# Kernel optimization log

Measured on AMD Instinct MI355X. Metric: run time of the kernel, lower is better.

Reference implementation:

```python
import jax, jax.numpy as jnp
import numpy as np

H = 512      # hidden size
V = 10000    # input_output_size (vocab)
L = 32       # max_length
B = 256      # batch
SOS = 1


def setup_inputs() -> dict:
    key = jax.random.key(0)
    ks = jax.random.split(key, 20)
    g = lambda k, shape: jax.random.normal(k, shape, dtype=jnp.float32) * 0.05
    return dict(
        input_tensor=jax.random.randint(ks[0], (B, L), 0, V),
        target_tensor=jax.random.randint(ks[1], (B, L), 0, V),
        # encoder: embedding + GRU
        enc_embed=g(ks[2], (V, H)),
        enc_w_ih=g(ks[3], (3 * H, H)), enc_w_hh=g(ks[4], (3 * H, H)),
        enc_b_ih=g(ks[5], (3 * H,)), enc_b_hh=g(ks[6], (3 * H,)),
        # attention decoder: embedding + attn + attn_combine + GRU + out
        dec_embed=g(ks[7], (V, H)),
        attn_w=g(ks[8], (L, 2 * H)), attn_b=g(ks[9], (L,)),
        comb_w=g(ks[10], (H, 2 * H)), comb_b=g(ks[11], (H,)),
        dec_w_ih=g(ks[12], (3 * H, H)), dec_w_hh=g(ks[13], (3 * H, H)),
        dec_b_ih=g(ks[14], (3 * H,)), dec_b_hh=g(ks[15], (3 * H,)),
        out_w=g(ks[16], (V, H)), out_b=g(ks[17], (V,)),
    )


def _gru_step(x, h, w_ih, w_hh, b_ih, b_hh):
    # PyTorch GRUCell math. x, h: [B, H]
    gi = x @ w_ih.T + b_ih          # [B, 3H]
    gh = h @ w_hh.T + b_hh          # [B, 3H]
    i_r, i_z, i_n = jnp.split(gi, 3, axis=-1)
    h_r, h_z, h_n = jnp.split(gh, 3, axis=-1)
    r = jax.nn.sigmoid(i_r + h_r)
    z = jax.nn.sigmoid(i_z + h_z)
    n = jnp.tanh(i_n + r * h_n)
    return (1.0 - z) * n + z * h


def reference(input_tensor, target_tensor,
              enc_embed, enc_w_ih, enc_w_hh, enc_b_ih, enc_b_hh,
              dec_embed, attn_w, attn_b, comb_w, comb_b,
              dec_w_ih, dec_w_hh, dec_b_ih, dec_b_hh, out_w, out_b):
    inp_t = input_tensor.T   # [L, B]
    tgt_t = target_tensor.T  # [L, B]
    h0 = jnp.zeros((B, H), dtype=enc_embed.dtype)

    # ---- encoder: scan over time ----
    def enc_step(h, tok):
        x = enc_embed[tok]  # [B, H]
        h2 = _gru_step(x, h, enc_w_ih, enc_w_hh, enc_b_ih, enc_b_hh)
        return h2, h2       # encoder output == hidden

    enc_hidden, enc_outs = jax.lax.scan(enc_step, h0, inp_t)  # enc_outs: [L, B, H]

    # ---- decoder with teacher forcing (phase='train', ratio=1.0) ----
    sos = jnp.full((1, B), SOS, dtype=tgt_t.dtype)
    dec_inputs = jnp.concatenate([sos, tgt_t[:-1]], axis=0)  # [L, B]

    def dec_step(h, tok):
        emb = dec_embed[tok]                                   # [B, H]
        aw = jax.nn.softmax(jnp.concatenate([emb, h], axis=-1) @ attn_w.T + attn_b)  # [B, L]
        applied = jnp.einsum('bl,lbh->bh', aw, enc_outs)       # attention over encoder outputs
        x = jax.nn.relu(jnp.concatenate([emb, applied], axis=-1) @ comb_w.T + comb_b)
        h2 = _gru_step(x, h, dec_w_ih, dec_w_hh, dec_b_ih, dec_b_hh)
        logits = jax.nn.log_softmax(h2 @ out_w.T + out_b)      # [B, V]
        return h2, logits

    _, network_outputs = jax.lax.scan(dec_step, enc_hidden, dec_inputs)  # [L, B, V]
    return network_outputs
```

## Files before the change

### kernel.cpp

```cpp
#include <hip/hip_runtime.h>

#define HD 512
#define VOC 10000
#define SL 32
#define BA 256
#define BH (BA*HD)

typedef __bf16 b16x8 __attribute__((ext_vector_type(8)));
typedef float f32x4 __attribute__((ext_vector_type(4)));
typedef unsigned u32x4 __attribute__((ext_vector_type(4)));

__device__ __forceinline__ ushort f2bf(float x) {
  unsigned u = __float_as_uint(x);
  u += 0x7fffu + ((u >> 16) & 1u);
  return (ushort)(u >> 16);
}

__device__ __forceinline__ void stg_sc(void* p, u32x4 v) {
  asm volatile("global_store_dwordx4 %0, %1, off sc0 sc1"
               :: "v"(p), "v"(v) : "memory");
}
__device__ __forceinline__ void stg_sc1(void* p, unsigned v) {
  asm volatile("global_store_dword %0, %1, off sc0 sc1"
               :: "v"(p), "v"(v) : "memory");
}
__device__ __forceinline__ void stg_plain(void* p, unsigned v) {
  asm volatile("global_store_dword %0, %1, off"
               :: "v"(p), "v"(v) : "memory");
}
__device__ __forceinline__ unsigned ldg_sc0(const void* p) {
  unsigned v;
  asm volatile("global_load_dword %0, %1, off sc0"
               : "=v"(v) : "v"(p) : "memory");
  asm volatile("s_waitcnt vmcnt(0)" ::: "memory");
  return v;
}
__device__ __forceinline__ unsigned ldg_sc1(const void* p) {
  unsigned v;
  asm volatile("global_load_dword %0, %1, off sc0 sc1"
               : "=v"(v) : "v"(p) : "memory");
  asm volatile("s_waitcnt vmcnt(0)" ::: "memory");
  return v;
}
__device__ __forceinline__ void vmwait0() {
  asm volatile("s_waitcnt vmcnt(0)" ::: "memory");
  __builtin_amdgcn_sched_barrier(0);
}

__global__ __launch_bounds__(256) void cvt3_k(
    const float* __restrict__ w_out, ushort* __restrict__ o_out,
    const float* __restrict__ w_comb, ushort* __restrict__ o_comb,
    const float* __restrict__ w_attn, ushort* __restrict__ o_attn) {
  int b = blockIdx.x;
  const float* in; ushort* out; int i; int n4;
  if (b < 5000)      { in = w_out;  out = o_out;  i = b * 256 + threadIdx.x;          n4 = 1280000; }
  else if (b < 5512) { in = w_comb; out = o_comb; i = (b - 5000) * 256 + threadIdx.x; n4 = 131072; }
  else               { in = w_attn; out = o_attn; i = (b - 5512) * 256 + threadIdx.x; n4 = 8192; }
  if (i < n4) {
    float4 v = ((const float4*)in)[i];
    ((ushort4*)out)[i] = make_ushort4(f2bf(v.x), f2bf(v.y), f2bf(v.z), f2bf(v.w));
  }
}

__global__ __launch_bounds__(64) void gather2_k(
    const float* __restrict__ enc_t, const float* __restrict__ dec_t,
    const int* __restrict__ in_tok, const int* __restrict__ tgt_tok,
    ushort* __restrict__ enc_o, ushort* __restrict__ dec_o) {
  int bid = blockIdx.x;
  int isDec = bid >= SL * BA;
  int row = isDec ? bid - SL * BA : bid;
  int l = row >> 8, b = row & 255;
  int tok = isDec ? ((l == 0) ? 1 : tgt_tok[b * SL + l - 1]) : in_tok[b * SL + l];
  const float* table = isDec ? dec_t : enc_t;
  ushort* out = isDec ? dec_o : enc_o;
  const float4* src = (const float4*)(table + (size_t)tok * HD);
  int t = threadIdx.x;
  float4 v0 = src[t * 2], v1 = src[t * 2 + 1];
  uint4 o;
  o.x = (unsigned)f2bf(v0.x) | ((unsigned)f2bf(v0.y) << 16);
  o.y = (unsigned)f2bf(v0.z) | ((unsigned)f2bf(v0.w) << 16);
  o.z = (unsigned)f2bf(v1.x) | ((unsigned)f2bf(v1.y) << 16);
  o.w = (unsigned)f2bf(v1.z) | ((unsigned)f2bf(v1.w) << 16);
  *(uint4*)(out + (size_t)row * HD + t * 8) = o;
}

__global__ __launch_bounds__(256) void gemm_k(
    const ushort* __restrict__ A, const ushort* __restrict__ W,
    int N, int ldw, const float* __restrict__ bias,
    float* __restrict__ outf, int ldc) {
  __shared__ ushort lsA[4][64][8];
  __shared__ ushort lsB[4][64][8];
  __shared__ float ctile[64][68];
  int t = threadIdx.x;
  int lane = t & 63, w = t >> 6;
  int m0 = blockIdx.x * 64, n0 = blockIdx.y * 64;
  f32x4 acc[4] = {};
  int sr = t >> 2, g = t & 3;
  const ushort* Ap = A + (size_t)(m0 + sr) * HD + g * 8;
  int nr = n0 + sr; if (nr > N - 1) nr = N - 1;
  const ushort* Wp = W + (size_t)nr * ldw + g * 8;
  for (int ks = 0; ks < 16; ++ks) {
    *(uint4*)(&lsA[g][sr][0]) = *(const uint4*)(Ap + ks * 32);
    *(uint4*)(&lsB[g][sr][0]) = *(const uint4*)(Wp + ks * 32);
    __syncthreads();
    int gg = lane >> 4, r = lane & 15;
    b16x8 bf = *(const b16x8*)(&lsB[gg][w * 16 + r][0]);
#pragma unroll
    for (int mi = 0; mi < 4; ++mi) {
      b16x8 af = *(const b16x8*)(&lsA[gg][mi * 16 + r][0]);
      acc[mi] = __builtin_amdgcn_mfma_f32_16x16x32_bf16(af, bf, acc[mi], 0, 0, 0);
    }
    __syncthreads();
  }
  int gg = lane >> 4, cl = lane & 15;
  int tcol = w * 16 + cl;
  int bc = n0 + tcol; if (bc > N - 1) bc = N - 1;
  float bv = bias ? bias[bc] : 0.f;
#pragma unroll
  for (int mi = 0; mi < 4; ++mi)
#pragma unroll
    for (int r = 0; r < 4; ++r)
      ctile[mi * 16 + gg * 4 + r][tcol] = acc[mi][r] + bv;
  __syncthreads();
  int row = t >> 2, q = t & 3;
#pragma unroll
  for (int j = 0; j < 4; ++j) {
    int c = q * 16 + j * 4;
    if (n0 + c + 3 <= N - 1)
      *(float4*)(outf + (size_t)(m0 + row) * ldc + n0 + c) =
          *(const float4*)&ctile[row][c];
  }
}

__global__ __launch_bounds__(256) void gemmW_k(
    const ushort* __restrict__ A, const ushort* __restrict__ W,
    ushort* __restrict__ outS) {
  __shared__ ushort lsA[4][64][8];
  __shared__ ushort lsB[4][64][8];
  __shared__ ushort ctileS[64][64];
  int t = threadIdx.x, lane = t & 63, w = t >> 6;
  int m0 = blockIdx.x * 64, n0 = blockIdx.y * 64;
  f32x4 acc[4] = {};
  int sr = t >> 2, g = t & 3;
  const ushort* Ap = A + (size_t)(m0 + sr) * HD + g * 8;
  const ushort* Wp = W + (size_t)(n0 + sr) * 1024 + 512 + g * 8;
  for (int ks = 0; ks < 16; ++ks) {
    *(uint4*)(&lsA[g][sr][0]) = *(const uint4*)(Ap + ks * 32);
    *(uint4*)(&lsB[g][sr][0]) = *(const uint4*)(Wp + ks * 32);
    __syncthreads();
    int gg = lane >> 4, r = lane & 15;
    b16x8 bf = *(const b16x8*)(&lsB[gg][w * 16 + r][0]);
#pragma unroll
    for (int mi = 0; mi < 4; ++mi) {
      b16x8 af = *(const b16x8*)(&lsA[gg][mi * 16 + r][0]);
      acc[mi] = __builtin_amdgcn_mfma_f32_16x16x32_bf16(af, bf, acc[mi], 0, 0, 0);
    }
    __syncthreads();
  }
  int gg = lane >> 4, cl = lane & 15;
  int tcol = w * 16 + cl;
#pragma unroll
  for (int mi = 0; mi < 4; ++mi)
#pragma unroll
    for (int r = 0; r < 4; ++r)
      ctileS[mi * 16 + gg * 4 + r][tcol] = f2bf(acc[mi][r]);
  __syncthreads();
  int l = m0 >> 8, b0 = m0 & 255;
  int sl_i = t >> 6, tid = t & 63;
  ushort* dst = outS + (((size_t)l * 32 + (n0 >> 4) + sl_i) * 256 + b0 + tid) * 16;
  *(uint4*)dst = *(const uint4*)&ctileS[tid][sl_i * 16];
  *(uint4*)(dst + 8) = *(const uint4*)&ctileS[tid][sl_i * 16 + 8];
}

__global__ __launch_bounds__(256) void gemm128_k(
    const ushort* __restrict__ A, const ushort* __restrict__ W,
    int N, const float* __restrict__ bias,
    float* __restrict__ outf, int ldc) {
  __shared__ ushort lsA[4][128][8];
  __shared__ ushort lsB[4][64][8];
  __shared__ float ctile[128][68];
  int t = threadIdx.x, lane = t & 63, w = t >> 6;
  int m0 = blockIdx.x * 128, n0 = blockIdx.y * 64;
  f32x4 acc[8] = {};
  int arow = t >> 1, ag = t & 1;
  const ushort* Ap = A + (size_t)(m0 + arow) * HD + ag * 16;
  int brow = t >> 2, bg = t & 3;
  int nr = n0 + brow; if (nr > N - 1) nr = N - 1;
  const ushort* Wp = W + (size_t)nr * HD + bg * 8;
  for (int ks = 0; ks < 16; ++ks) {
    *(uint4*)(&lsA[ag * 2][arow][0])     = *(const uint4*)(Ap + ks * 32);
    *(uint4*)(&lsA[ag * 2 + 1][arow][0]) = *(const uint4*)(Ap + ks * 32 + 8);
    *(uint4*)(&lsB[bg][brow][0])         = *(const uint4*)(Wp + ks * 32);
    __syncthreads();
    int gg = lane >> 4, r = lane & 15;
    b16x8 bf = *(const b16x8*)(&lsB[gg][w * 16 + r][0]);
#pragma unroll
    for (int mi = 0; mi < 8; ++mi) {
      b16x8 af = *(const b16x8*)(&lsA[gg][mi * 16 + r][0]);
      acc[mi] = __builtin_amdgcn_mfma_f32_16x16x32_bf16(af, bf, acc[mi], 0, 0, 0);
    }
    __syncthreads();
  }
  int gg = lane >> 4, cl = lane & 15;
  int tcol = w * 16 + cl;
  int bc = n0 + tcol; if (bc > N - 1) bc = N - 1;
  float bv = bias[bc];
#pragma unroll
  for (int mi = 0; mi < 8; ++mi)
#pragma unroll
    for (int r = 0; r < 4; ++r)
      ctile[mi * 16 + gg * 4 + r][tcol] = acc[mi][r] + bv;
  __syncthreads();
  int row = t >> 1, hf = t & 1;
#pragma unroll
  for (int j = 0; j < 8; ++j) {
    int c = hf * 32 + j * 4;
    if (n0 + c + 3 <= N - 1)
      *(float4*)(outf + (size_t)(m0 + row) * ldc + n0 + c) =
          *(const float4*)&ctile[row][c];
  }
}


__device__ __forceinline__ const ushort* sfrag(const ushort* base, int kh,
                                               int gg, int row) {
  return base + (kh * 16 + (gg >> 1)) * 4096 + row * 16 + (gg & 1) * 8;
}

template <bool XS>
__device__ __forceinline__ void gru_phase(
    int r0, int sl, int lane, int w, int t,
    const ushort* __restrict__ x_src, const ushort* __restrict__ h_src,
    const ushort (*Wlds)[2][8][64][8],
    const float* __restrict__ b_ih, const float* __restrict__ b_hh,
    float* hp, ushort* __restrict__ hbf_dst, ushort* __restrict__ hrm_dst,
    float (*red)[6][64][4], ushort (*stile)[16]) {
  int mf = w & 1, kh = w >> 1;
  int lr = lane & 15, gg = lane >> 4;
  int row_a = r0 + mf * 16 + lr;
  b16x8 xa[8], ha[8];
  if (XS) {
    const ushort* xr = sfrag(x_src, kh, gg, row_a);
#pragma unroll
    for (int ks = 0; ks < 8; ++ks) xa[ks] = *(const b16x8*)(xr + ks * 8192);
  } else {
    const ushort* xr = x_src + (size_t)row_a * HD + kh * 256 + gg * 8;
#pragma unroll
    for (int ks = 0; ks < 8; ++ks) xa[ks] = *(const b16x8*)(xr + ks * 32);
  }
  if (h_src) {
    const ushort* hr = sfrag(h_src, kh, gg, row_a);
#pragma unroll
    for (int ks = 0; ks < 8; ++ks) ha[ks] = *(const b16x8*)(hr + ks * 8192);
  } else {
#pragma unroll
    for (int ks = 0; ks < 8; ++ks) ha[ks] = b16x8{};
  }
  f32x4 acc[6] = {};
#pragma unroll
  for (int ks = 0; ks < 8; ++ks) {
#pragma unroll
    for (int g3 = 0; g3 < 3; ++g3) {
      b16x8 bi = *(const b16x8*)(&Wlds[g3][kh][ks][lane][0]);
      b16x8 bh = *(const b16x8*)(&Wlds[3 + g3][kh][ks][lane][0]);
      acc[g3] = __builtin_amdgcn_mfma_f32_16x16x32_bf16(xa[ks], bi, acc[g3], 0, 0, 0);
      acc[3 + g3] = __builtin_amdgcn_mfma_f32_16x16x32_bf16(ha[ks], bh, acc[3 + g3], 0, 0, 0);
    }
  }
  if (kh == 1) {
#pragma unroll
    for (int s = 0; s < 6; ++s) *(f32x4*)&red[mf][s][lane][0] = acc[s];
  }
  __syncthreads();
  if (kh == 0) {
    int j = sl * 16 + lr;
#pragma unroll
    for (int s = 0; s < 6; ++s) acc[s] += *(const f32x4*)&red[mf][s][lane][0];
    float bir = b_ih[j], biz = b_ih[512 + j], bin_ = b_ih[1024 + j];
    float bhr = b_hh[j], bhz = b_hh[512 + j], bhn = b_hh[1024 + j];
#pragma unroll
    for (int ri = 0; ri < 4; ++ri) {
      float ir = acc[0][ri] + bir, iz = acc[1][ri] + biz, inn = acc[2][ri] + bin_;
      float hr2 = acc[3][ri] + bhr, hz = acc[4][ri] + bhz, hn = acc[5][ri] + bhn;
      float rr = 1.f / (1.f + expf(-(ir + hr2)));
      float zz = 1.f / (1.f + expf(-(iz + hz)));
      float nn = tanhf(inn + rr * hn);
      float h2 = (1.f - zz) * nn + zz * hp[ri];
      hp[ri] = h2;
      stile[mf * 16 + gg * 4 + ri][lr] = f2bf(h2);
    }
  }
  __syncthreads();
  if (t < 64) {
    stg_sc(hbf_dst + sl * 4096 + r0 * 16 + t * 8, ((const u32x4*)stile)[t]);
    int row = t >> 1, c = t & 1;
    *(uint4*)(hrm_dst + (size_t)(r0 + row) * HD + sl * 16 + c * 8) =
        *(const uint4*)&stile[row][c * 8];
  }
}

__device__ __forceinline__ void attnx_phase(
    int r0, int sl, int lane, int w, int t, int l,
    const ushort* __restrict__ h_bf, const ushort* __restrict__ attn_w_bf,
    const float* __restrict__ attn_pre, const ushort* __restrict__ encW,
    const float* __restrict__ comb_pre, ushort* __restrict__ x_dst,
    float (*sS)[32][33], float (*sAW)[33], ushort (*stile)[16]) {
  int mf = w & 1, kh = w >> 1;
  int lr = lane & 15, gg = lane >> 4;
  int row_a = r0 + mf * 16 + lr;
  const ushort* hr = sfrag(h_bf, kh, gg, row_a);
  const ushort* w0 = attn_w_bf + (size_t)lr * 1024 + 512 + kh * 256 + gg * 8;
  const ushort* w1 = attn_w_bf + (size_t)(16 + lr) * 1024 + 512 + kh * 256 + gg * 8;
  f32x4 a0 = {}, a1 = {};
#pragma unroll
  for (int ks = 0; ks < 8; ++ks) {
    b16x8 ah = *(const b16x8*)(hr + ks * 8192);
    b16x8 b0 = *(const b16x8*)(w0 + ks * 32);
    b16x8 b1 = *(const b16x8*)(w1 + ks * 32);
    a0 = __builtin_amdgcn_mfma_f32_16x16x32_bf16(ah, b0, a0, 0, 0, 0);
    a1 = __builtin_amdgcn_mfma_f32_16x16x32_bf16(ah, b1, a1, 0, 0, 0);
  }
#pragma unroll
  for (int ri = 0; ri < 4; ++ri) {
    sS[kh][mf * 16 + gg * 4 + ri][lr] = a0[ri];
    sS[kh][mf * 16 + gg * 4 + ri][16 + lr] = a1[ri];
  }
  __syncthreads();
  int r = t >> 3, q = t & 7;
  float4 pre = *(const float4*)(attn_pre + ((size_t)l * BA + r0 + r) * 32 + q * 4);
  float v0 = sS[0][r][q * 4 + 0] + sS[1][r][q * 4 + 0] + pre.x;
  float v1 = sS[0][r][q * 4 + 1] + sS[1][r][q * 4 + 1] + pre.y;
  float v2 = sS[0][r][q * 4 + 2] + sS[1][r][q * 4 + 2] + pre.z;
  float v3 = sS[0][r][q * 4 + 3] + sS[1][r][q * 4 + 3] + pre.w;
  float mx = fmaxf(fmaxf(v0, v1), fmaxf(v2, v3));
  for (int o = 1; o < 8; o <<= 1) mx = fmaxf(mx, __shfl_xor(mx, o, 64));
  float e0 = expf(v0 - mx), e1 = expf(v1 - mx), e2 = expf(v2 - mx), e3 = expf(v3 - mx);
  float s = e0 + e1 + e2 + e3;
  for (int o = 1; o < 8; o <<= 1) s += __shfl_xor(s, o, 64);
  float inv = 1.f / s;
  sAW[r][q * 4 + 0] = e0 * inv; sAW[r][q * 4 + 1] = e1 * inv;
  sAW[r][q * 4 + 2] = e2 * inv; sAW[r][q * 4 + 3] = e3 * inv;
  __syncthreads();
  int rr = t >> 3, dp = t & 7;
  const float* cp = comb_pre + ((size_t)l * BA + r0 + rr) * HD + sl * 16 + dp * 2;
  float f0 = cp[0], f1 = cp[1];
  const ushort* ep = encW + sl * 4096 + (r0 + rr) * 16 + dp * 2;
#pragma unroll 8
  for (int ll = 0; ll < 32; ++ll) {
    float aw = sAW[rr][ll];
    unsigned u = *(const unsigned*)(ep + (size_t)ll * BH);
    f0 += aw * __uint_as_float(u << 16);
    f1 += aw * __uint_as_float(u & 0xffff0000u);
  }
  f0 = fmaxf(f0, 0.f); f1 = fmaxf(f1, 0.f);
  unsigned ov = (unsigned)f2bf(f0) | ((unsigned)f2bf(f1) << 16);
  *(unsigned*)&stile[rr][dp * 2] = ov;
  __syncthreads();
  if (t < 64)
    stg_sc(x_dst + sl * 4096 + r0 * 16 + t * 8, ((const u32x4*)stile)[t]);
}

struct EncArgs {
  const ushort* enc_emb_bf;
  const float* enc_w_ih; const float* enc_w_hh;
  const float* enc_b_ih; const float* enc_b_hh;
  ushort* enc_outs_s;
  ushort* enc_outs_rm;
  float* Hc;
  unsigned* fL2; unsigned* fLLC;
};

struct DecArgs {
  const float* dec_w_ih; const float* dec_w_hh;
  const float* dec_b_ih; const float* dec_b_hh;
  const ushort* attn_w_bf;
  const float* attn_pre;
  const float* comb_pre;
  const ushort* enc_outs_s;
  const ushort* encW;
  const float* Hc;
  ushort* H2_s; ushort* H2_rm; ushort* x_s;
  unsigned* fL2; unsigned* fLLC;
};

union DScr {
  float red[2][6][64][4];
  struct { float sS[2][32][33]; float sAW[32][33]; } at;
};

#define GSYNC_DEF(fL2p, fLLCp)                                          \
  auto gsync = [&]() {                                                  \
    ++sync_idx;                                                         \
    __syncthreads();                                                    \
    if (w == 0) {                                                       \
      vmwait0();                                                        \
      if (lane == 0) {                                                  \
        stg_plain(&(fL2p)[sl * 4], sync_idx);                           \
        stg_sc1(&(fLLCp)[sl * 16], sync_idx);                           \
      }                                                                 \
      int it = 0;                                                       \
      for (;;) {                                                        \
        unsigned v = ldg_sc0(&(fL2p)[(lane & 31) * 4]);                 \
        if (!__any(v < sync_idx)) break;                                \
        if ((++it & 3) == 0) {                                          \
          unsigned v2 = ldg_sc1(&(fLLCp)[(lane & 31) * 16]);            \
          if (!__any(v < sync_idx && v2 < sync_idx)) break;             \
        }                                                               \
        __builtin_amdgcn_s_sleep(1);                                    \
      }                                                                 \
    }                                                                   \
    __syncthreads();                                                    \
  }

#define LOAD_GRU_W32(Wih, Whh)                                          \
  for (int c = w; c < 96; c += 4) {                                     \
    int g = c >> 4, rem = c & 15, kh2 = rem >> 3, ks = rem & 7;         \
    const float* src = (g < 3) ? (Wih) : (Whh);                         \
    int gr = (g % 3) * 512 + sl * 16 + (lane & 15);                     \
    int col = kh2 * 256 + ks * 32 + (lane >> 4) * 8;                    \
    const float4* s4 = (const float4*)(src + (size_t)gr * HD + col);    \
    float4 va = s4[0], vb = s4[1];                                      \
    uint4 o;                                                            \
    o.x = (unsigned)f2bf(va.x) | ((unsigned)f2bf(va.y) << 16);          \
    o.y = (unsigned)f2bf(va.z) | ((unsigned)f2bf(va.w) << 16);          \
    o.z = (unsigned)f2bf(vb.x) | ((unsigned)f2bf(vb.y) << 16);          \
    o.w = (unsigned)f2bf(vb.z) | ((unsigned)f2bf(vb.w) << 16);          \
    *(uint4*)&Wlds[g][kh2][ks][lane][0] = o;                            \
  }

__global__ __launch_bounds__(256) void enc_k(EncArgs a) {
  __shared__ ushort Wlds[6][2][8][64][8];
  __shared__ float red[2][6][64][4];
  __shared__ ushort stile[32][16];
  int bid = blockIdx.x;
  int rg = bid & 7, sl = bid >> 3;
  int t = threadIdx.x, lane = t & 63, w = t >> 6;
  int r0 = rg * 32;
  unsigned* fL2 = a.fL2 + rg * 32 * 4;
  unsigned* fLLC = a.fLLC + rg * 32 * 16;
  unsigned sync_idx = 0;
  GSYNC_DEF(fL2, fLLC);

  LOAD_GRU_W32(a.enc_w_ih, a.enc_w_hh);
  __syncthreads();

  float hp[4] = {0.f, 0.f, 0.f, 0.f};
  for (int l = 0; l < SL; ++l) {
    gru_phase<false>(r0, sl, lane, w, t,
                     a.enc_emb_bf + (size_t)l * BH,
                     l ? a.enc_outs_s + (size_t)(l - 1) * BH : nullptr,
                     Wlds, a.enc_b_ih, a.enc_b_hh,
                     hp, a.enc_outs_s + (size_t)l * BH,
                     a.enc_outs_rm + (size_t)l * BH, red, stile);
    if (l != SL - 1) gsync();
  }
  if ((w >> 1) == 0) {
    int mf2 = w & 1, gg2 = lane >> 4, j = sl * 16 + (lane & 15);
#pragma unroll
    for (int ri = 0; ri < 4; ++ri)
      a.Hc[(size_t)(r0 + mf2 * 16 + gg2 * 4 + ri) * HD + j] = hp[ri];
  }
}

__global__ __launch_bounds__(256) void dec_k(DecArgs a) {
  __shared__ ushort Wlds[6][2][8][64][8];
  __shared__ DScr scr;
  __shared__ ushort stile[32][16];
  int bid = blockIdx.x;
  int rg = bid & 7, sl = bid >> 3;
  int t = threadIdx.x, lane = t & 63, w = t >> 6;
  int r0 = rg * 32;
  unsigned* fL2 = a.fL2 + rg * 32 * 4;
  unsigned* fLLC = a.fLLC + rg * 32 * 16;
  unsigned sync_idx = 0;
  GSYNC_DEF(fL2, fLLC);

  LOAD_GRU_W32(a.dec_w_ih, a.dec_w_hh);

  float hp[4] = {0.f, 0.f, 0.f, 0.f};
  if ((w >> 1) == 0) {
    int mf2 = w & 1, gg2 = lane >> 4, j = sl * 16 + (lane & 15);
#pragma unroll
    for (int ri = 0; ri < 4; ++ri)
      hp[ri] = a.Hc[(size_t)(r0 + mf2 * 16 + gg2 * 4 + ri) * HD + j];
  }
  __syncthreads();

  for (int l = 0; l < SL; ++l) {
    const ushort* h_bf = l ? a.H2_s + (size_t)(l - 1) * BH
                           : a.enc_outs_s + (size_t)31 * BH;
    attnx_phase(r0, sl, lane, w, t, l, h_bf, a.attn_w_bf, a.attn_pre,
                a.encW, a.comb_pre, a.x_s + (size_t)l * BH,
                scr.at.sS, scr.at.sAW, stile);
    gsync();
    gru_phase<true>(r0, sl, lane, w, t, a.x_s + (size_t)l * BH, h_bf,
                    Wlds, a.dec_b_ih, a.dec_b_hh,
                    hp, a.H2_s + (size_t)l * BH,
                    a.H2_rm + (size_t)l * BH, scr.red, stile);
    if (l != SL - 1) gsync();
  }
}

__global__ __launch_bounds__(256) void lsesub_k(float* __restrict__ logits) {
  __shared__ float redm[4], reds[4];
  int row = blockIdx.x, t = threadIdx.x;
  float4* p = (float4*)(logits + (size_t)row * VOC);
  float4 v[10];
  float m = -1e30f, s = 0.f;
#pragma unroll
  for (int j = 0; j < 10; ++j) {
    int i = t + j * 256;
    if (i < 2500) {
      v[j] = p[i];
      float mx = fmaxf(fmaxf(v[j].x, v[j].y), fmaxf(v[j].z, v[j].w));
      if (mx > m) { s *= expf(m - mx); m = mx; }
      s += expf(v[j].x - m) + expf(v[j].y - m) + expf(v[j].z - m) + expf(v[j].w - m);
    }
  }
#pragma unroll
  for (int o = 32; o; o >>= 1) {
    float m2 = __shfl_xor(m, o, 64), s2 = __shfl_xor(s, o, 64);
    float mn = fmaxf(m, m2);
    s = s * expf(m - mn) + s2 * expf(m2 - mn);
    m = mn;
  }
  if ((t & 63) == 0) { redm[t >> 6] = m; reds[t >> 6] = s; }
  __syncthreads();
  float mf = fmaxf(fmaxf(redm[0], redm[1]), fmaxf(redm[2], redm[3]));
  float sf = reds[0] * expf(redm[0] - mf) + reds[1] * expf(redm[1] - mf) +
             reds[2] * expf(redm[2] - mf) + reds[3] * expf(redm[3] - mf);
  float z = mf + logf(sf);
#pragma unroll
  for (int j = 0; j < 10; ++j) {
    int i = t + j * 256;
    if (i < 2500) {
      v[j].x -= z; v[j].y -= z; v[j].z -= z; v[j].w -= z;
      p[i] = v[j];
    }
  }
}

extern "C" void kernel_launch(void* const* d_in, const int* in_sizes, int n_in,
                              void* d_out, int out_size, void* d_ws, size_t ws_size,
                              hipStream_t stream) {
  (void)in_sizes; (void)n_in; (void)out_size; (void)ws_size;
  const int* in_tok = (const int*)d_in[0];
  const int* tgt_tok = (const int*)d_in[1];
  const float* enc_embed = (const float*)d_in[2];
  const float* enc_w_ih = (const float*)d_in[3];
  const float* enc_w_hh = (const float*)d_in[4];
  const float* enc_b_ih = (const float*)d_in[5];
  const float* enc_b_hh = (const float*)d_in[6];
  const float* dec_embed = (const float*)d_in[7];
  const float* attn_w = (const float*)d_in[8];
  const float* attn_b = (const float*)d_in[9];
  const float* comb_w = (const float*)d_in[10];
  const float* comb_b = (const float*)d_in[11];
  const float* dec_w_ih = (const float*)d_in[12];
  const float* dec_w_hh = (const float*)d_in[13];
  const float* dec_b_ih = (const float*)d_in[14];
  const float* dec_b_hh = (const float*)d_in[15];
  const float* out_w = (const float*)d_in[16];
  const float* out_b = (const float*)d_in[17];
  float* out = (float*)d_out;

  char* ws = (char*)d_ws;
  size_t off = 0;
  auto carve = [&](size_t bytes) {
    void* p = ws + off;
    off += (bytes + 255) & ~(size_t)255;
    return p;
  };
  ushort* comb_w_bf  = (ushort*)carve(512 * 1024 * 2);
  ushort* attn_w_bf  = (ushort*)carve(32 * 1024 * 2);
  ushort* out_w_bf   = (ushort*)carve((size_t)VOC * HD * 2);
  ushort* enc_emb_bf = (ushort*)carve((size_t)SL * BA * HD * 2);
  ushort* dec_emb_bf = (ushort*)carve((size_t)SL * BA * HD * 2);
  float* attn_pre    = (float*)carve((size_t)SL * BA * 32 * 4);
  float* comb_pre    = (float*)carve((size_t)SL * BA * HD * 4);
  ushort* enc_outs_s = (ushort*)carve((size_t)SL * BA * HD * 2);
  ushort* enc_outs_rm= (ushort*)carve((size_t)SL * BA * HD * 2);
  ushort* encW       = (ushort*)carve((size_t)SL * BA * HD * 2);
  ushort* H2_s       = (ushort*)carve((size_t)SL * BA * HD * 2);
  ushort* H2_rm      = (ushort*)carve((size_t)SL * BA * HD * 2);
  ushort* x_s        = (ushort*)carve((size_t)SL * BA * HD * 2);
  float* Hc          = (float*)carve((size_t)BA * HD * 4);
  unsigned* fE_L2    = (unsigned*)carve(8 * 32 * 4 * 4);
  unsigned* fE_LLC   = (unsigned*)carve(8 * 32 * 16 * 4);
  unsigned* fD_L2    = (unsigned*)carve(8 * 32 * 4 * 4);
  unsigned* fD_LLC   = (unsigned*)carve(8 * 32 * 16 * 4);

  hipMemsetAsync(fE_L2, 0, (8 * 32 * 4 + 8 * 32 * 16) * 2 * 4, stream);
  cvt3_k<<<5544, 256, 0, stream>>>(out_w, out_w_bf, comb_w, comb_w_bf,
                                   attn_w, attn_w_bf);
  gather2_k<<<2 * SL * BA, 64, 0, stream>>>(enc_embed, dec_embed, in_tok,
                                            tgt_tok, enc_emb_bf, dec_emb_bf);

  gemm_k<<<dim3(128, 1), 256, 0, stream>>>(dec_emb_bf, attn_w_bf, 32, 1024,
                                           attn_b, attn_pre, 32);
  gemm_k<<<dim3(128, 8), 256, 0, stream>>>(dec_emb_bf, comb_w_bf, 512, 1024,
                                           comb_b, comb_pre, 512);

  EncArgs ea;
  ea.enc_emb_bf = enc_emb_bf;
  ea.enc_w_ih = enc_w_ih; ea.enc_w_hh = enc_w_hh;
  ea.enc_b_ih = enc_b_ih; ea.enc_b_hh = enc_b_hh;
  ea.enc_outs_s = enc_outs_s;
  ea.enc_outs_rm = enc_outs_rm;
  ea.Hc = Hc;
  ea.fL2 = fE_L2; ea.fLLC = fE_LLC;
  void* ekargs[] = { (void*)&ea };
  hipError_t ce = hipLaunchCooperativeKernel(enc_k, dim3(256), dim3(256),
                                             ekargs, 0, stream);
  if (ce != hipSuccess) enc_k<<<256, 256, 0, stream>>>(ea);

  gemmW_k<<<dim3(128, 8), 256, 0, stream>>>(enc_outs_rm, comb_w_bf, encW);

  DecArgs da;
  da.dec_w_ih = dec_w_ih; da.dec_w_hh = dec_w_hh;
  da.dec_b_ih = dec_b_ih; da.dec_b_hh = dec_b_hh;
  da.attn_w_bf = attn_w_bf;
  da.attn_pre = attn_pre;
  da.comb_pre = comb_pre;
  da.enc_outs_s = enc_outs_s;
  da.encW = encW;
  da.Hc = Hc;
  da.H2_s = H2_s; da.H2_rm = H2_rm; da.x_s = x_s;
  da.fL2 = fD_L2; da.fLLC = fD_LLC;
  void* dkargs[] = { (void*)&da };
  ce = hipLaunchCooperativeKernel(dec_k, dim3(256), dim3(256),
                                  dkargs, 0, stream);
  if (ce != hipSuccess) dec_k<<<256, 256, 0, stream>>>(da);

  gemm128_k<<<dim3(64, 157), 256, 0, stream>>>(H2_rm, out_w_bf, VOC,
                                               out_b, out, VOC);
  lsesub_k<<<SL * BA, 256, 0, stream>>>(out);
}
```

Baseline: 893.4 us.

## Split grid barriers into produce/await and overlap independent GEMMs with waits

Replaces the monolithic grid sync with separate produce/await halves so each block can start work that does not depend on other blocks before it waits. In the encoder the input-side GRU GEMM runs before waiting on the previous hidden state. In the decoder the hidden-side GRU GEMM and the encW loads run before their waits. encW is re-laid out so each thread's 32 encoder timesteps are contiguous and can be prefetched into registers, and the two precompute GEMMs are merged into one launch. This cuts barrier stall time on the serial recurrence at the cost of more register pressure.

```diff
diff --git a/kernel.cpp b/kernel.cpp
--- a/kernel.cpp
+++ b/kernel.cpp
@@ -84,21 +84,26 @@
   *(uint4*)(out + (size_t)row * HD + t * 8) = o;
 }
 
-__global__ __launch_bounds__(256) void gemm_k(
-    const ushort* __restrict__ A, const ushort* __restrict__ W,
-    int N, int ldw, const float* __restrict__ bias,
-    float* __restrict__ outf, int ldc) {
+__global__ __launch_bounds__(256) void gemm2_k(
+    const ushort* __restrict__ A,
+    const ushort* __restrict__ Wc, const ushort* __restrict__ Wa,
+    const float* __restrict__ bc, const float* __restrict__ ba,
+    float* __restrict__ outc, float* __restrict__ outa) {
   __shared__ ushort lsA[4][64][8];
   __shared__ ushort lsB[4][64][8];
   __shared__ float ctile[64][68];
   int t = threadIdx.x;
   int lane = t & 63, w = t >> 6;
-  int m0 = blockIdx.x * 64, n0 = blockIdx.y * 64;
+  int by = blockIdx.y;
+  const ushort* W; const float* bias; float* outf; int N, n0, ldc;
+  if (by < 8) { W = Wc; bias = bc; outf = outc; N = 512; n0 = by * 64; ldc = 512; }
+  else        { W = Wa; bias = ba; outf = outa; N = 32;  n0 = 0;       ldc = 32; }
+  int m0 = blockIdx.x * 64;
   f32x4 acc[4] = {};
   int sr = t >> 2, g = t & 3;
   const ushort* Ap = A + (size_t)(m0 + sr) * HD + g * 8;
   int nr = n0 + sr; if (nr > N - 1) nr = N - 1;
-  const ushort* Wp = W + (size_t)nr * ldw + g * 8;
+  const ushort* Wp = W + (size_t)nr * 1024 + g * 8;
   for (int ks = 0; ks < 16; ++ks) {
     *(uint4*)(&lsA[g][sr][0]) = *(const uint4*)(Ap + ks * 32);
     *(uint4*)(&lsB[g][sr][0]) = *(const uint4*)(Wp + ks * 32);
@@ -114,8 +119,8 @@
   }
   int gg = lane >> 4, cl = lane & 15;
   int tcol = w * 16 + cl;
-  int bc = n0 + tcol; if (bc > N - 1) bc = N - 1;
-  float bv = bias ? bias[bc] : 0.f;
+  int bc2 = n0 + tcol; if (bc2 > N - 1) bc2 = N - 1;
+  float bv = bias[bc2];
 #pragma unroll
   for (int mi = 0; mi < 4; ++mi)
 #pragma unroll
@@ -134,7 +139,7 @@
 
 __global__ __launch_bounds__(256) void gemmW_k(
     const ushort* __restrict__ A, const ushort* __restrict__ W,
-    ushort* __restrict__ outS) {
+    ushort* __restrict__ outI) {
   __shared__ ushort lsA[4][64][8];
   __shared__ ushort lsB[4][64][8];
   __shared__ ushort ctileS[64][64];
@@ -167,7 +172,8 @@
   __syncthreads();
   int l = m0 >> 8, b0 = m0 & 255;
   int sl_i = t >> 6, tid = t & 63;
-  ushort* dst = outS + (((size_t)l * 32 + (n0 >> 4) + sl_i) * 256 + b0 + tid) * 16;
+  int sl_g = (n0 >> 4) + sl_i;
+  ushort* dst = outI + ((((size_t)sl_g * 256 + b0 + tid) * 32) + l) * 16;
   *(uint4*)dst = *(const uint4*)&ctileS[tid][sl_i * 16];
   *(uint4*)(dst + 8) = *(const uint4*)&ctileS[tid][sl_i * 16 + 8];
 }
@@ -227,139 +233,6 @@
   return base + (kh * 16 + (gg >> 1)) * 4096 + row * 16 + (gg & 1) * 8;
 }
 
-template <bool XS>
-__device__ __forceinline__ void gru_phase(
-    int r0, int sl, int lane, int w, int t,
-    const ushort* __restrict__ x_src, const ushort* __restrict__ h_src,
-    const ushort (*Wlds)[2][8][64][8],
-    const float* __restrict__ b_ih, const float* __restrict__ b_hh,
-    float* hp, ushort* __restrict__ hbf_dst, ushort* __restrict__ hrm_dst,
-    float (*red)[6][64][4], ushort (*stile)[16]) {
-  int mf = w & 1, kh = w >> 1;
-  int lr = lane & 15, gg = lane >> 4;
-  int row_a = r0 + mf * 16 + lr;
-  b16x8 xa[8], ha[8];
-  if (XS) {
-    const ushort* xr = sfrag(x_src, kh, gg, row_a);
-#pragma unroll
-    for (int ks = 0; ks < 8; ++ks) xa[ks] = *(const b16x8*)(xr + ks * 8192);
-  } else {
-    const ushort* xr = x_src + (size_t)row_a * HD + kh * 256 + gg * 8;
-#pragma unroll
-    for (int ks = 0; ks < 8; ++ks) xa[ks] = *(const b16x8*)(xr + ks * 32);
-  }
-  if (h_src) {
-    const ushort* hr = sfrag(h_src, kh, gg, row_a);
-#pragma unroll
-    for (int ks = 0; ks < 8; ++ks) ha[ks] = *(const b16x8*)(hr + ks * 8192);
-  } else {
-#pragma unroll
-    for (int ks = 0; ks < 8; ++ks) ha[ks] = b16x8{};
-  }
-  f32x4 acc[6] = {};
-#pragma unroll
-  for (int ks = 0; ks < 8; ++ks) {
-#pragma unroll
-    for (int g3 = 0; g3 < 3; ++g3) {
-      b16x8 bi = *(const b16x8*)(&Wlds[g3][kh][ks][lane][0]);
-      b16x8 bh = *(const b16x8*)(&Wlds[3 + g3][kh][ks][lane][0]);
-      acc[g3] = __builtin_amdgcn_mfma_f32_16x16x32_bf16(xa[ks], bi, acc[g3], 0, 0, 0);
-      acc[3 + g3] = __builtin_amdgcn_mfma_f32_16x16x32_bf16(ha[ks], bh, acc[3 + g3], 0, 0, 0);
-    }
-  }
-  if (kh == 1) {
-#pragma unroll
-    for (int s = 0; s < 6; ++s) *(f32x4*)&red[mf][s][lane][0] = acc[s];
-  }
-  __syncthreads();
-  if (kh == 0) {
-    int j = sl * 16 + lr;
-#pragma unroll
-    for (int s = 0; s < 6; ++s) acc[s] += *(const f32x4*)&red[mf][s][lane][0];
-    float bir = b_ih[j], biz = b_ih[512 + j], bin_ = b_ih[1024 + j];
-    float bhr = b_hh[j], bhz = b_hh[512 + j], bhn = b_hh[1024 + j];
-#pragma unroll
-    for (int ri = 0; ri < 4; ++ri) {
-      float ir = acc[0][ri] + bir, iz = acc[1][ri] + biz, inn = acc[2][ri] + bin_;
-      float hr2 = acc[3][ri] + bhr, hz = acc[4][ri] + bhz, hn = acc[5][ri] + bhn;
-      float rr = 1.f / (1.f + expf(-(ir + hr2)));
-      float zz = 1.f / (1.f + expf(-(iz + hz)));
-      float nn = tanhf(inn + rr * hn);
-      float h2 = (1.f - zz) * nn + zz * hp[ri];
-      hp[ri] = h2;
-      stile[mf * 16 + gg * 4 + ri][lr] = f2bf(h2);
-    }
-  }
-  __syncthreads();
-  if (t < 64) {
-    stg_sc(hbf_dst + sl * 4096 + r0 * 16 + t * 8, ((const u32x4*)stile)[t]);
-    int row = t >> 1, c = t & 1;
-    *(uint4*)(hrm_dst + (size_t)(r0 + row) * HD + sl * 16 + c * 8) =
-        *(const uint4*)&stile[row][c * 8];
-  }
-}
-
-__device__ __forceinline__ void attnx_phase(
-    int r0, int sl, int lane, int w, int t, int l,
-    const ushort* __restrict__ h_bf, const ushort* __restrict__ attn_w_bf,
-    const float* __restrict__ attn_pre, const ushort* __restrict__ encW,
-    const float* __restrict__ comb_pre, ushort* __restrict__ x_dst,
-    float (*sS)[32][33], float (*sAW)[33], ushort (*stile)[16]) {
-  int mf = w & 1, kh = w >> 1;
-  int lr = lane & 15, gg = lane >> 4;
-  int row_a = r0 + mf * 16 + lr;
-  const ushort* hr = sfrag(h_bf, kh, gg, row_a);
-  const ushort* w0 = attn_w_bf + (size_t)lr * 1024 + 512 + kh * 256 + gg * 8;
-  const ushort* w1 = attn_w_bf + (size_t)(16 + lr) * 1024 + 512 + kh * 256 + gg * 8;
-  f32x4 a0 = {}, a1 = {};
-#pragma unroll
-  for (int ks = 0; ks < 8; ++ks) {
-    b16x8 ah = *(const b16x8*)(hr + ks * 8192);
-    b16x8 b0 = *(const b16x8*)(w0 + ks * 32);
-    b16x8 b1 = *(const b16x8*)(w1 + ks * 32);
-    a0 = __builtin_amdgcn_mfma_f32_16x16x32_bf16(ah, b0, a0, 0, 0, 0);
-    a1 = __builtin_amdgcn_mfma_f32_16x16x32_bf16(ah, b1, a1, 0, 0, 0);
-  }
-#pragma unroll
-  for (int ri = 0; ri < 4; ++ri) {
-    sS[kh][mf * 16 + gg * 4 + ri][lr] = a0[ri];
-    sS[kh][mf * 16 + gg * 4 + ri][16 + lr] = a1[ri];
-  }
-  __syncthreads();
-  int r = t >> 3, q = t & 7;
-  float4 pre = *(const float4*)(attn_pre + ((size_t)l * BA + r0 + r) * 32 + q * 4);
-  float v0 = sS[0][r][q * 4 + 0] + sS[1][r][q * 4 + 0] + pre.x;
-  float v1 = sS[0][r][q * 4 + 1] + sS[1][r][q * 4 + 1] + pre.y;
-  float v2 = sS[0][r][q * 4 + 2] + sS[1][r][q * 4 + 2] + pre.z;
-  float v3 = sS[0][r][q * 4 + 3] + sS[1][r][q * 4 + 3] + pre.w;
-  float mx = fmaxf(fmaxf(v0, v1), fmaxf(v2, v3));
-  for (int o = 1; o < 8; o <<= 1) mx = fmaxf(mx, __shfl_xor(mx, o, 64));
-  float e0 = expf(v0 - mx), e1 = expf(v1 - mx), e2 = expf(v2 - mx), e3 = expf(v3 - mx);
-  float s = e0 + e1 + e2 + e3;
-  for (int o = 1; o < 8; o <<= 1) s += __shfl_xor(s, o, 64);
-  float inv = 1.f / s;
-  sAW[r][q * 4 + 0] = e0 * inv; sAW[r][q * 4 + 1] = e1 * inv;
-  sAW[r][q * 4 + 2] = e2 * inv; sAW[r][q * 4 + 3] = e3 * inv;
-  __syncthreads();
-  int rr = t >> 3, dp = t & 7;
-  const float* cp = comb_pre + ((size_t)l * BA + r0 + rr) * HD + sl * 16 + dp * 2;
-  float f0 = cp[0], f1 = cp[1];
-  const ushort* ep = encW + sl * 4096 + (r0 + rr) * 16 + dp * 2;
-#pragma unroll 8
-  for (int ll = 0; ll < 32; ++ll) {
-    float aw = sAW[rr][ll];
-    unsigned u = *(const unsigned*)(ep + (size_t)ll * BH);
-    f0 += aw * __uint_as_float(u << 16);
-    f1 += aw * __uint_as_float(u & 0xffff0000u);
-  }
-  f0 = fmaxf(f0, 0.f); f1 = fmaxf(f1, 0.f);
-  unsigned ov = (unsigned)f2bf(f0) | ((unsigned)f2bf(f1) << 16);
-  *(unsigned*)&stile[rr][dp * 2] = ov;
-  __syncthreads();
-  if (t < 64)
-    stg_sc(x_dst + sl * 4096 + r0 * 16 + t * 8, ((const u32x4*)stile)[t]);
-}
-
 struct EncArgs {
   const ushort* enc_emb_bf;
   const float* enc_w_ih; const float* enc_w_hh;
@@ -388,23 +261,26 @@
   struct { float sS[2][32][33]; float sAW[32][33]; } at;
 };
 
-#define GSYNC_DEF(fL2p, fLLCp)                                          \
-  auto gsync = [&]() {                                                  \
-    ++sync_idx;                                                         \
+#define BAR_DEFS(fL2p, fLLCp)                                           \
+  auto produce = [&](unsigned val) {                                    \
     __syncthreads();                                                    \
     if (w == 0) {                                                       \
       vmwait0();                                                        \
       if (lane == 0) {                                                  \
-        stg_plain(&(fL2p)[sl * 4], sync_idx);                           \
-        stg_sc1(&(fLLCp)[sl * 16], sync_idx);                           \
+        stg_plain(&(fL2p)[sl * 4], val);                                \
+        stg_sc1(&(fLLCp)[sl * 16], val);                                \
       }                                                                 \
+    }                                                                   \
+  };                                                                    \
+  auto await = [&](unsigned val) {                                      \
+    if (w == 0) {                                                       \
       int it = 0;                                                       \
       for (;;) {                                                        \
         unsigned v = ldg_sc0(&(fL2p)[(lane & 31) * 4]);                 \
-        if (!__any(v < sync_idx)) break;                                \
+        if (!__any(v < val)) break;                                     \
         if ((++it & 3) == 0) {                                          \
           unsigned v2 = ldg_sc1(&(fLLCp)[(lane & 31) * 16]);            \
-          if (!__any(v < sync_idx && v2 < sync_idx)) break;             \
+          if (!__any(v < val && v2 < val)) break;                       \
         }                                                               \
         __builtin_amdgcn_s_sleep(1);                                    \
       }                                                                 \
@@ -428,37 +304,100 @@
     *(uint4*)&Wlds[g][kh2][ks][lane][0] = o;                            \
   }
 
+#define GRU_TAIL(b_ih_, b_hh_, hbf_dst_, hrm_dst_)                      \
+  if (kh == 1) {                                                        \
+    _Pragma("unroll")                                                   \
+    for (int s = 0; s < 6; ++s) *(f32x4*)&redp[mf][s][lane][0] = acc[s];\
+  }                                                                     \
+  __syncthreads();                                                      \
+  if (kh == 0) {                                                        \
+    int j = sl * 16 + lr;                                               \
+    _Pragma("unroll")                                                   \
+    for (int s = 0; s < 6; ++s) acc[s] += *(const f32x4*)&redp[mf][s][lane][0]; \
+    float bir = (b_ih_)[j], biz = (b_ih_)[512 + j], bin_ = (b_ih_)[1024 + j]; \
+    float bhr = (b_hh_)[j], bhz = (b_hh_)[512 + j], bhn = (b_hh_)[1024 + j]; \
+    _Pragma("unroll")                                                   \
+    for (int ri = 0; ri < 4; ++ri) {                                    \
+      float ir = acc[0][ri] + bir, iz = acc[1][ri] + biz, inn = acc[2][ri] + bin_; \
+      float hr2 = acc[3][ri] + bhr, hz = acc[4][ri] + bhz, hn = acc[5][ri] + bhn; \
+      float rrg = 1.f / (1.f + expf(-(ir + hr2)));                      \
+      float zz = 1.f / (1.f + expf(-(iz + hz)));                        \
+      float nn = tanhf(inn + rrg * hn);                                 \
+      float h2 = (1.f - zz) * nn + zz * hp[ri];                         \
+      hp[ri] = h2;                                                      \
+      stile[mf * 16 + gg * 4 + ri][lr] = f2bf(h2);                      \
+    }                                                                   \
+  }                                                                     \
+  __syncthreads();                                                      \
+  if (t < 64) {                                                         \
+    stg_sc((hbf_dst_) + sl * 4096 + r0 * 16 + t * 8, ((const u32x4*)stile)[t]); \
+    if (hrm_dst_) {                                                     \
+      int row2 = t >> 1, c2 = t & 1;                                    \
+      *(uint4*)((hrm_dst_) + (size_t)(r0 + row2) * HD + sl * 16 + c2 * 8) = \
+          *(const uint4*)&stile[row2][c2 * 8];                          \
+    }                                                                   \
+  }
+
 __global__ __launch_bounds__(256) void enc_k(EncArgs a) {
   __shared__ ushort Wlds[6][2][8][64][8];
   __shared__ float red[2][6][64][4];
   __shared__ ushort stile[32][16];
+  float (*redp)[6][64][4] = red;
   int bid = blockIdx.x;
   int rg = bid & 7, sl = bid >> 3;
   int t = threadIdx.x, lane = t & 63, w = t >> 6;
   int r0 = rg * 32;
   unsigned* fL2 = a.fL2 + rg * 32 * 4;
   unsigned* fLLC = a.fLLC + rg * 32 * 16;
-  unsigned sync_idx = 0;
-  GSYNC_DEF(fL2, fLLC);
+  BAR_DEFS(fL2, fLLC);
 
   LOAD_GRU_W32(a.enc_w_ih, a.enc_w_hh);
   __syncthreads();
 
+  int mf = w & 1, kh = w >> 1;
+  int lr = lane & 15, gg = lane >> 4;
+  int row_a = r0 + mf * 16 + lr;
   float hp[4] = {0.f, 0.f, 0.f, 0.f};
+
   for (int l = 0; l < SL; ++l) {
-    gru_phase<false>(r0, sl, lane, w, t,
-                     a.enc_emb_bf + (size_t)l * BH,
-                     l ? a.enc_outs_s + (size_t)(l - 1) * BH : nullptr,
-                     Wlds, a.enc_b_ih, a.enc_b_hh,
-                     hp, a.enc_outs_s + (size_t)l * BH,
-                     a.enc_outs_rm + (size_t)l * BH, red, stile);
-    if (l != SL - 1) gsync();
+    const ushort* xr = a.enc_emb_bf + (size_t)l * BH + (size_t)row_a * HD +
+                       kh * 256 + gg * 8;
+    b16x8 xa[8];
+#pragma unroll
+    for (int ks = 0; ks < 8; ++ks) xa[ks] = *(const b16x8*)(xr + ks * 32);
+    f32x4 acc[6] = {};
+#pragma unroll
+    for (int ks = 0; ks < 8; ++ks)
+#pragma unroll
+      for (int g3 = 0; g3 < 3; ++g3)
+        acc[g3] = __builtin_amdgcn_mfma_f32_16x16x32_bf16(
+            xa[ks], *(const b16x8*)(&Wlds[g3][kh][ks][lane][0]), acc[g3], 0, 0, 0);
+    if (l) await((unsigned)l);
+    b16x8 ha[8];
+    if (l) {
+      const ushort* hr = sfrag(a.enc_outs_s + (size_t)(l - 1) * BH, kh, gg, row_a);
+#pragma unroll
+      for (int ks = 0; ks < 8; ++ks) ha[ks] = *(const b16x8*)(hr + ks * 8192);
+    } else {
+#pragma unroll
+      for (int ks = 0; ks < 8; ++ks) ha[ks] = b16x8{};
+    }
+#pragma unroll
+    for (int ks = 0; ks < 8; ++ks)
+#pragma unroll
+      for (int g3 = 0; g3 < 3; ++g3)
+        acc[3 + g3] = __builtin_amdgcn_mfma_f32_16x16x32_bf16(
+            ha[ks], *(const b16x8*)(&Wlds[3 + g3][kh][ks][lane][0]),
+            acc[3 + g3], 0, 0, 0);
+    GRU_TAIL(a.enc_b_ih, a.enc_b_hh, a.enc_outs_s + (size_t)l * BH,
+             a.enc_outs_rm + (size_t)l * BH);
+    if (l != SL - 1) produce((unsigned)(l + 1));
   }
   if ((w >> 1) == 0) {
-    int mf2 = w & 1, gg2 = lane >> 4, j = sl * 16 + (lane & 15);
+    int j = sl * 16 + lr;
 #pragma unroll
     for (int ri = 0; ri < 4; ++ri)
-      a.Hc[(size_t)(r0 + mf2 * 16 + gg2 * 4 + ri) * HD + j] = hp[ri];
+      a.Hc[(size_t)(r0 + mf * 16 + gg * 4 + ri) * HD + j] = hp[ri];
   }
 }
 
@@ -466,38 +405,128 @@
   __shared__ ushort Wlds[6][2][8][64][8];
   __shared__ DScr scr;
   __shared__ ushort stile[32][16];
+  float (*redp)[6][64][4] = scr.red;
   int bid = blockIdx.x;
   int rg = bid & 7, sl = bid >> 3;
   int t = threadIdx.x, lane = t & 63, w = t >> 6;
   int r0 = rg * 32;
   unsigned* fL2 = a.fL2 + rg * 32 * 4;
   unsigned* fLLC = a.fLLC + rg * 32 * 16;
-  unsigned sync_idx = 0;
-  GSYNC_DEF(fL2, fLLC);
+  BAR_DEFS(fL2, fLLC);
 
   LOAD_GRU_W32(a.dec_w_ih, a.dec_w_hh);
+
+  int mf = w & 1, kh = w >> 1;
+  int lr = lane & 15, gg = lane >> 4;
+  int row_a = r0 + mf * 16 + lr;
+  int rr = t >> 3, dp = t & 7;
 
   float hp[4] = {0.f, 0.f, 0.f, 0.f};
   if ((w >> 1) == 0) {
-    int mf2 = w & 1, gg2 = lane >> 4, j = sl * 16 + (lane & 15);
+    int j = sl * 16 + lr;
 #pragma unroll
     for (int ri = 0; ri < 4; ++ri)
-      hp[ri] = a.Hc[(size_t)(r0 + mf2 * 16 + gg2 * 4 + ri) * HD + j];
+      hp[ri] = a.Hc[(size_t)(r0 + mf * 16 + gg * 4 + ri) * HD + j];
   }
   __syncthreads();
 
   for (int l = 0; l < SL; ++l) {
     const ushort* h_bf = l ? a.H2_s + (size_t)(l - 1) * BH
                            : a.enc_outs_s + (size_t)31 * BH;
-    attnx_phase(r0, sl, lane, w, t, l, h_bf, a.attn_w_bf, a.attn_pre,
-                a.encW, a.comb_pre, a.x_s + (size_t)l * BH,
-                scr.at.sS, scr.at.sAW, stile);
-    gsync();
-    gru_phase<true>(r0, sl, lane, w, t, a.x_s + (size_t)l * BH, h_bf,
-                    Wlds, a.dec_b_ih, a.dec_b_hh,
-                    hp, a.H2_s + (size_t)l * BH,
-                    a.H2_rm + (size_t)l * BH, scr.red, stile);
-    if (l != SL - 1) gsync();
+    unsigned ev[32];
+    {
+      const ushort* ep = a.encW + (((size_t)sl * 256 + r0 + rr) * 32) * 16 + dp * 2;
+#pragma unroll
+      for (int ll = 0; ll < 32; ++ll)
+        ev[ll] = *(const unsigned*)(ep + ll * 16);
+    }
+    if (l) await(2u * l);
+    {
+      const ushort* hr = sfrag(h_bf, kh, gg, row_a);
+      const ushort* w0 = a.attn_w_bf + (size_t)lr * 1024 + 512 + kh * 256 + gg * 8;
+      const ushort* w1 = a.attn_w_bf + (size_t)(16 + lr) * 1024 + 512 + kh * 256 + gg * 8;
+      f32x4 a0 = {}, a1 = {};
+#pragma unroll
+      for (int ks = 0; ks < 8; ++ks) {
+        b16x8 ah = *(const b16x8*)(hr + ks * 8192);
+        a0 = __builtin_amdgcn_mfma_f32_16x16x32_bf16(
+            ah, *(const b16x8*)(w0 + ks * 32), a0, 0, 0, 0);
+        a1 = __builtin_amdgcn_mfma_f32_16x16x32_bf16(
+            ah, *(const b16x8*)(w1 + ks * 32), a1, 0, 0, 0);
+      }
+#pragma unroll
+      for (int ri = 0; ri < 4; ++ri) {
+        scr.at.sS[kh][mf * 16 + gg * 4 + ri][lr] = a0[ri];
+        scr.at.sS[kh][mf * 16 + gg * 4 + ri][16 + lr] = a1[ri];
+      }
+    }
+    __syncthreads();
+    {
+      float4 pre = *(const float4*)(a.attn_pre + ((size_t)l * BA + r0 + rr) * 32 + dp * 4);
+      float v0 = scr.at.sS[0][rr][dp * 4 + 0] + scr.at.sS[1][rr][dp * 4 + 0] + pre.x;
+      float v1 = scr.at.sS[0][rr][dp * 4 + 1] + scr.at.sS[1][rr][dp * 4 + 1] + pre.y;
+      float v2 = scr.at.sS[0][rr][dp * 4 + 2] + scr.at.sS[1][rr][dp * 4 + 2] + pre.z;
+      float v3 = scr.at.sS[0][rr][dp * 4 + 3] + scr.at.sS[1][rr][dp * 4 + 3] + pre.w;
+      float mx = fmaxf(fmaxf(v0, v1), fmaxf(v2, v3));
+      for (int o = 1; o < 8; o <<= 1) mx = fmaxf(mx, __shfl_xor(mx, o, 64));
+      float e0 = expf(v0 - mx), e1 = expf(v1 - mx);
+      float e2 = expf(v2 - mx), e3 = expf(v3 - mx);
+      float s = e0 + e1 + e2 + e3;
+      for (int o = 1; o < 8; o <<= 1) s += __shfl_xor(s, o, 64);
+      float inv = 1.f / s;
+      scr.at.sAW[rr][dp * 4 + 0] = e0 * inv; scr.at.sAW[rr][dp * 4 + 1] = e1 * inv;
+      scr.at.sAW[rr][dp * 4 + 2] = e2 * inv; scr.at.sAW[rr][dp * 4 + 3] = e3 * inv;
+    }
+    __syncthreads();
+    {
+      const float* cp = a.comb_pre + ((size_t)l * BA + r0 + rr) * HD + sl * 16 + dp * 2;
+      float f0 = cp[0], f1 = cp[1];
+#pragma unroll
+      for (int ll = 0; ll < 32; ++ll) {
+        float aw = scr.at.sAW[rr][ll];
+        f0 += aw * __uint_as_float(ev[ll] << 16);
+        f1 += aw * __uint_as_float(ev[ll] & 0xffff0000u);
+      }
+      f0 = fmaxf(f0, 0.f); f1 = fmaxf(f1, 0.f);
+      *(unsigned*)&stile[rr][dp * 2] =
+          (unsigned)f2bf(f0) | ((unsigned)f2bf(f1) << 16);
+    }
+    __syncthreads();
+    if (t < 64)
+      stg_sc(a.x_s + (size_t)l * BH + sl * 4096 + r0 * 16 + t * 8,
+             ((const u32x4*)stile)[t]);
+    produce(2u * l + 1);
+    f32x4 acc[6] = {};
+    {
+      const ushort* hr = sfrag(h_bf, kh, gg, row_a);
+      b16x8 ha[8];
+#pragma unroll
+      for (int ks = 0; ks < 8; ++ks) ha[ks] = *(const b16x8*)(hr + ks * 8192);
+#pragma unroll
+      for (int ks = 0; ks < 8; ++ks)
+#pragma unroll
+        for (int g3 = 0; g3 < 3; ++g3)
+          acc[3 + g3] = __builtin_amdgcn_mfma_f32_16x16x32_bf16(
+              ha[ks], *(const b16x8*)(&Wlds[3 + g3][kh][ks][lane][0]),
+              acc[3 + g3], 0, 0, 0);
+    }
+    await(2u * l + 1);
+    {
+      const ushort* xr = sfrag(a.x_s + (size_t)l * BH, kh, gg, row_a);
+      b16x8 xa[8];
+#pragma unroll
+      for (int ks = 0; ks < 8; ++ks) xa[ks] = *(const b16x8*)(xr + ks * 8192);
+#pragma unroll
+      for (int ks = 0; ks < 8; ++ks)
+#pragma unroll
+        for (int g3 = 0; g3 < 3; ++g3)
+          acc[g3] = __builtin_amdgcn_mfma_f32_16x16x32_bf16(
+              xa[ks], *(const b16x8*)(&Wlds[g3][kh][ks][lane][0]),
+              acc[g3], 0, 0, 0);
+    }
+    GRU_TAIL(a.dec_b_ih, a.dec_b_hh, a.H2_s + (size_t)l * BH,
+             a.H2_rm + (size_t)l * BH);
+    if (l != SL - 1) produce(2u * l + 2);
   }
 }
 
@@ -596,10 +625,8 @@
   gather2_k<<<2 * SL * BA, 64, 0, stream>>>(enc_embed, dec_embed, in_tok,
                                             tgt_tok, enc_emb_bf, dec_emb_bf);
 
-  gemm_k<<<dim3(128, 1), 256, 0, stream>>>(dec_emb_bf, attn_w_bf, 32, 1024,
-                                           attn_b, attn_pre, 32);
-  gemm_k<<<dim3(128, 8), 256, 0, stream>>>(dec_emb_bf, comb_w_bf, 512, 1024,
-                                           comb_b, comb_pre, 512);
+  gemm2_k<<<dim3(128, 9), 256, 0, stream>>>(dec_emb_bf, comb_w_bf, attn_w_bf,
+                                            comb_b, attn_b, comb_pre, attn_pre);
 
   EncArgs ea;
   ea.enc_emb_bf = enc_emb_bf;
```

New measurement: 856.5 us. 1.04x faster.
